# Kernel optimization log

Measured on AMD Instinct MI355X. Metric: run time of the kernel, lower is better.

Reference implementation:

```python
import jax, jax.numpy as jnp
import numpy as np

M = 100        # n_models
D = 16         # input_dim
H = 128        # hidden_dim
O = 1          # output_dim
NH = 4         # n_hidden
N = 16384      # batch of query points


def setup_inputs() -> dict:
    key = jax.random.key(0)
    ks = jax.random.split(key, 9)
    s = 0.1
    return {
        "x": jax.random.normal(ks[0], (N, D), dtype=jnp.float32),
        "W1": jax.random.normal(ks[1], (M, H, D), dtype=jnp.float32) * s,
        "b1": jax.random.normal(ks[2], (M, H), dtype=jnp.float32) * s,
        "Wh": jax.random.normal(ks[3], (M, NH, H, H), dtype=jnp.float32) * s,
        "bh": jax.random.normal(ks[4], (M, NH, H), dtype=jnp.float32) * s,
        "Wmu": jax.random.normal(ks[5], (M, O, H), dtype=jnp.float32) * s,
        "bmu": jax.random.normal(ks[6], (M, O), dtype=jnp.float32) * s,
        "Wsig": jax.random.normal(ks[7], (M, O, H), dtype=jnp.float32) * s,
        "bsig": jax.random.normal(ks[8], (M, O), dtype=jnp.float32) * s,
    }


def reference(x, W1, b1, Wh, bh, Wmu, bmu, Wsig, bsig):
    # Batched across all M models: h has shape [M, N, H]
    h = jax.nn.relu(jnp.einsum("nd,mhd->mnh", x, W1) + b1[:, None, :])
    for i in range(NH):  # fixed small structural loop over hidden layers
        h = jax.nn.relu(jnp.einsum("mnh,mkh->mnk", h, Wh[:, i]) + bh[:, i][:, None, :])
    mu = jnp.einsum("mnh,moh->mno", h, Wmu) + bmu[:, None, :]      # [M, N, O]
    sigma = jnp.exp(jnp.einsum("mnh,moh->mno", h, Wsig) + bsig[:, None, :])
    return (mu, sigma)
```

## Files before the change

### kernel.cpp

```cpp
#include <hip/hip_runtime.h>


typedef float  f32x4  __attribute__((ext_vector_type(4)));
typedef float  f32x16 __attribute__((ext_vector_type(16)));
typedef __bf16 bf16x4 __attribute__((ext_vector_type(4)));
typedef __bf16 bf16x8 __attribute__((ext_vector_type(8)));
typedef short  s16x4  __attribute__((ext_vector_type(4)));

union BF4  { bf16x4 v; uint2 u2; };
union FRAG { bf16x8 v; uint4 u4; };
union PKW  { uint2 u2; s16x4 s4; };

#define MODELS 100
#define NPT    16384
#define HDIM   128
#define SG_OFF (MODELS * NPT)

#define XB_OFF   0
#define W1B_OFF  262144
#define WHB_OFF  466944
#define WMU_OFF  7020544
#define WSG_OFF  7033344

#define GTOT 880768

__global__ __launch_bounds__(256) void cvt_weights(
    const float* __restrict__ x,   const float* __restrict__ W1,
    const float* __restrict__ Wh,  const float* __restrict__ Wmu,
    const float* __restrict__ Wsg, unsigned short* __restrict__ ws)
{
  int gid = blockIdx.x * 256 + threadIdx.x;
  if (gid >= GTOT) return;
  const float* src;
  unsigned int dst;
  if (gid < 32768) {
    src = x + gid * 8;                       dst = XB_OFF + gid * 8;
  } else if (gid < 58368) {
    int g = gid - 32768;
    src = W1 + g * 8;                        dst = W1B_OFF + g * 8;
  } else if (gid < 877568) {
    int g = gid - 58368;
    int chunk  = g >> 11;
    int within = g & 2047;
    int r   = within >> 4;
    int col = ((within & 15) * 8) ^ ((r & 15) << 3);
    src = Wh + (size_t)g * 8;
    dst = WHB_OFF + chunk * 16384 + r * HDIM + col;
  } else if (gid < 879168) {
    int g = gid - 877568;
    src = Wmu + g * 8;                       dst = WMU_OFF + g * 8;
  } else {
    int g = gid - 879168;
    src = Wsg + g * 8;                       dst = WSG_OFF + g * 8;
  }
  f32x4 a = *(const f32x4*)src;
  f32x4 b = *(const f32x4*)(src + 4);
  BF4 lo, hi;
  lo.v = __builtin_convertvector(a, bf16x4);
  hi.v = __builtin_convertvector(b, bf16x4);
  uint4 u; u.x = lo.u2.x; u.y = lo.u2.y; u.z = hi.u2.x; u.w = hi.u2.y;
  *(uint4*)&ws[dst] = u;
}

__device__ __forceinline__ void gload_lds16(const void* g, void* l) {
  __builtin_amdgcn_global_load_lds(
      (const __attribute__((address_space(1))) void*)g,
      (__attribute__((address_space(3))) void*)l, 16, 0, 0);
}

#define MFMA32(A,B,C) __builtin_amdgcn_mfma_f32_32x32x16_bf16((A),(B),(C),0,0,0)

__device__ __forceinline__ void build_hfrag(const f32x16 (&acc)[2][4],
                                            uint4 (&hf)[2][8]) {
  const s16x4 z4 = {0, 0, 0, 0};
  #pragma unroll
  for (int nt = 0; nt < 2; ++nt) {
    #pragma unroll
    for (int kt2 = 0; kt2 < 4; ++kt2) {
      uint2 P[4];
      #pragma unroll
      for (int q = 0; q < 4; ++q) {
        f32x4 v;
        v[0] = acc[nt][kt2][4*q+0]; v[1] = acc[nt][kt2][4*q+1];
        v[2] = acc[nt][kt2][4*q+2]; v[3] = acc[nt][kt2][4*q+3];
        BF4 b; b.v = __builtin_convertvector(v, bf16x4);
        PKW p; p.u2 = b.u2;
        p.s4 = __builtin_elementwise_max(p.s4, z4);
        P[q] = p.u2;
      }
      #pragma unroll
      for (int sb = 0; sb < 2; ++sb) {
        unsigned int x0 = P[2*sb].x, y0 = P[2*sb+1].x;
        unsigned int x1 = P[2*sb].y, y1 = P[2*sb+1].y;
        asm("v_permlane32_swap_b32 %0, %1" : "+v"(x0), "+v"(y0));
        asm("v_permlane32_swap_b32 %0, %1" : "+v"(x1), "+v"(y1));
        uint4 f; f.x = x0; f.y = x1; f.z = y0; f.w = y1;
        hf[nt][2*kt2+sb] = f;
      }
    }
  }
}

__global__ __launch_bounds__(256, 2) void ens_mlp(
    const unsigned short* __restrict__ ws,
    const float* __restrict__ b1,  const float* __restrict__ bh,
    const float* __restrict__ bmu, const float* __restrict__ bsg,
    float* __restrict__ out)
{
  __shared__ unsigned short wlds[2][HDIM * HDIM];

  const int bid = blockIdx.x;
  const int swz = (bid & 7) * 800 + (bid >> 3);
  const int m   = swz >> 6;
  const int nb0 = (swz & 63) << 8;

  const int t    = threadIdx.x;
  const int lane = t & 63;
  const int wv   = t >> 6;
  const int l31  = lane & 31;
  const int hi   = lane >> 5;
  const int nbw  = nb0 + wv * 64;

  const unsigned short* whm = ws + WHB_OFF + m * 65536;

  #pragma unroll
  for (int b = 0; b < 2; ++b) {
    const char* src = (const char*)(whm + b * 16384);
    char* dst = (char*)wlds[b];
    #pragma unroll
    for (int it = 0; it < 8; ++it) {
      int off = t * 16 + it * 4096;
      gload_lds16(src + off, dst + off);
    }
  }

  uint4  hfrag[2][8];
  f32x16 acc[2][4];

  {
    const unsigned short* W1m = ws + W1B_OFF + m * (HDIM * 16);
    const unsigned short* xp  = ws + XB_OFF;
    FRAG w1f[4], xf[2];
    #pragma unroll
    for (int kt2 = 0; kt2 < 4; ++kt2)
      w1f[kt2].v = *(const bf16x8*)&W1m[(kt2 * 32 + l31) * 16 + hi * 8];
    #pragma unroll
    for (int nt = 0; nt < 2; ++nt)
      xf[nt].v = *(const bf16x8*)&xp[(nbw + nt * 32 + l31) * 16 + hi * 8];
    #pragma unroll
    for (int kt2 = 0; kt2 < 4; ++kt2) {
      union { f32x16 v; f32x4 q[4]; } C;
      #pragma unroll
      for (int q = 0; q < 4; ++q)
        C.q[q] = *(const f32x4*)(b1 + m * HDIM + kt2 * 32 + q * 8 + hi * 4);
      #pragma unroll
      for (int nt = 0; nt < 2; ++nt)
        acc[nt][kt2] = MFMA32(w1f[kt2].v, xf[nt].v, C.v);
    }
  }
  build_hfrag(acc, hfrag);

  __syncthreads();

  #pragma unroll
  for (int i = 0; i < 4; ++i) {
    const char* wl = (const char*)wlds[i & 1];
    const float* bp = bh + m * 512 + i * HDIM;

    union { f32x16 v; f32x4 q[4]; } C[4];
    #pragma unroll
    for (int kt2 = 0; kt2 < 4; ++kt2)
      #pragma unroll
      for (int q = 0; q < 4; ++q)
        C[kt2].q[q] = *(const f32x4*)(bp + kt2 * 32 + q * 8 + hi * 4);

    #pragma unroll
    for (int ks = 0; ks < 8; ++ks) {
      FRAG wf[4];
      #pragma unroll
      for (int kt2 = 0; kt2 < 4; ++kt2) {
        int off = (kt2 * 32 + l31) * 256 + ((ks * 32 + hi * 16) ^ ((l31 & 15) << 4));
        wf[kt2].u4 = *(const uint4*)(wl + off);
      }
      #pragma unroll
      for (int kt2 = 0; kt2 < 4; ++kt2)
        #pragma unroll
        for (int nt = 0; nt < 2; ++nt) {
          FRAG hv; hv.u4 = hfrag[nt][ks];
          acc[nt][kt2] = MFMA32(wf[kt2].v, hv.v,
                                ks == 0 ? C[kt2].v : acc[nt][kt2]);
        }
    }
    build_hfrag(acc, hfrag);

    if (i < 3) __syncthreads();
    if (i < 2) {
      const char* src = (const char*)(whm + (i + 2) * 16384);
      char* dst = (char*)wlds[i & 1];
      #pragma unroll
      for (int it = 0; it < 8; ++it) {
        int off = t * 16 + it * 4096;
        gload_lds16(src + off, dst + off);
      }
    }
  }

  {
    FRAG hw[8];
    const unsigned short* wp = ws + (l31 == 0 ? WMU_OFF : WSG_OFF) + m * HDIM;
    #pragma unroll
    for (int ks = 0; ks < 8; ++ks) {
      if (l31 < 2) {
        hw[ks].v = *(const bf16x8*)&wp[ks * 16 + hi * 8];
      } else {
        uint4 z; z.x = 0u; z.y = 0u; z.z = 0u; z.w = 0u;
        hw[ks].u4 = z;
      }
    }
    f32x16 C;
    #pragma unroll
    for (int j = 0; j < 16; ++j) C[j] = 0.0f;
    if (hi == 0) { C[0] = bmu[m]; C[1] = bsg[m]; }

    #pragma unroll
    for (int nt = 0; nt < 2; ++nt) {
      f32x16 a2;
      #pragma unroll
      for (int ks = 0; ks < 8; ++ks) {
        FRAG hv; hv.u4 = hfrag[nt][ks];
        a2 = MFMA32(hw[ks].v, hv.v, ks == 0 ? C : a2);
      }
      if (hi == 0) {
        int n = nbw + nt * 32 + l31;
        out[m * NPT + n]          = a2[0];
        out[SG_OFF + m * NPT + n] = expf(a2[1]);
      }
    }
  }
}

extern "C" void kernel_launch(void* const* d_in, const int* in_sizes, int n_in,
                              void* d_out, int out_size, void* d_ws, size_t ws_size,
                              hipStream_t stream) {
  const float* x   = (const float*)d_in[0];
  const float* W1  = (const float*)d_in[1];
  const float* b1  = (const float*)d_in[2];
  const float* Wh  = (const float*)d_in[3];
  const float* bh  = (const float*)d_in[4];
  const float* Wmu = (const float*)d_in[5];
  const float* bmu = (const float*)d_in[6];
  const float* Wsg = (const float*)d_in[7];
  const float* bsg = (const float*)d_in[8];
  unsigned short* ws = (unsigned short*)d_ws;
  (void)in_sizes; (void)n_in; (void)out_size; (void)ws_size;

  cvt_weights<<<(GTOT + 255) / 256, 256, 0, stream>>>(x, W1, Wh, Wmu, Wsg, ws);
  ens_mlp<<<6400, 256, 0, stream>>>(ws, b1, bh, bmu, bsg, (float*)d_out);
}
```

Before: 220.6 us.

## Keep all hidden-layer weights resident: 3/4 rows in LDS, last quarter in registers

Hidden weights are repacked so that rows 0-95 of every layer go to a contiguous LDS-friendly layout and rows 96-127 to a separate region. All four layers' LDS portions are loaded once at kernel start into 96 KB of shared memory, which removes the per-layer double-buffer reloads and their __syncthreads. The remaining quarter is loaded directly into registers and double-buffered by prefetching the next layer's slice. The cost is occupancy: launch bounds drop to one block per CU because of the larger LDS footprint and higher register use, which reduces latency hiding.

```diff
diff --git a/kernel.cpp b/kernel.cpp
--- a/kernel.cpp
+++ b/kernel.cpp
@@ -18,7 +18,8 @@
 
 #define XB_OFF   0
 #define W1B_OFF  262144
-#define WHB_OFF  466944
+#define WHL_OFF  466944
+#define WHG_OFF  5382144
 #define WMU_OFF  7020544
 #define WSG_OFF  7033344
 
@@ -42,10 +43,13 @@
     int g = gid - 58368;
     int chunk  = g >> 11;
     int within = g & 2047;
-    int r   = within >> 4;
-    int col = ((within & 15) * 8) ^ ((r & 15) << 3);
+    int r = within >> 4;
+    int j = within & 15;
     src = Wh + (size_t)g * 8;
-    dst = WHB_OFF + chunk * 16384 + r * HDIM + col;
+    if (r < 96)
+      dst = WHL_OFF + chunk * 12288 + (j * 96 + r) * 8;
+    else
+      dst = WHG_OFF + chunk * 4096  + (j * 32 + (r - 96)) * 8;
   } else if (gid < 879168) {
     int g = gid - 877568;
     src = Wmu + g * 8;                       dst = WMU_OFF + g * 8;
@@ -101,13 +105,13 @@
   }
 }
 
-__global__ __launch_bounds__(256, 2) void ens_mlp(
+__global__ __launch_bounds__(256, 1) void ens_mlp(
     const unsigned short* __restrict__ ws,
     const float* __restrict__ b1,  const float* __restrict__ bh,
     const float* __restrict__ bmu, const float* __restrict__ bsg,
     float* __restrict__ out)
 {
-  __shared__ unsigned short wlds[2][HDIM * HDIM];
+  __shared__ unsigned short wlds[4 * 12288];
 
   const int bid = blockIdx.x;
   const int swz = (bid & 7) * 800 + (bid >> 3);
@@ -121,14 +125,14 @@
   const int hi   = lane >> 5;
   const int nbw  = nb0 + wv * 64;
 
-  const unsigned short* whm = ws + WHB_OFF + m * 65536;
-
-  #pragma unroll
-  for (int b = 0; b < 2; ++b) {
-    const char* src = (const char*)(whm + b * 16384);
-    char* dst = (char*)wlds[b];
-    #pragma unroll
-    for (int it = 0; it < 8; ++it) {
+  const unsigned short* whl = ws + WHL_OFF + m * 49152;
+  const unsigned short* whg = ws + WHG_OFF + m * 16384;
+
+  {
+    const char* src = (const char*)whl;
+    char* dst = (char*)wlds;
+    #pragma unroll
+    for (int it = 0; it < 24; ++it) {
       int off = t * 16 + it * 4096;
       gload_lds16(src + off, dst + off);
     }
@@ -136,6 +140,11 @@
 
   uint4  hfrag[2][8];
   f32x16 acc[2][4];
+  FRAG   gw[2][8];
+
+  #pragma unroll
+  for (int ks = 0; ks < 8; ++ks)
+    gw[0][ks].u4 = *(const uint4*)&whg[((2 * ks + hi) * 32 + l31) * 8];
 
   {
     const unsigned short* W1m = ws + W1B_OFF + m * (HDIM * 16);
@@ -164,7 +173,14 @@
 
   #pragma unroll
   for (int i = 0; i < 4; ++i) {
-    const char* wl = (const char*)wlds[i & 1];
+    if (i < 3) {
+      const unsigned short* gsrc = whg + (i + 1) * 4096;
+      #pragma unroll
+      for (int ks = 0; ks < 8; ++ks)
+        gw[(i + 1) & 1][ks].u4 = *(const uint4*)&gsrc[((2 * ks + hi) * 32 + l31) * 8];
+    }
+
+    const char* wl = (const char*)wlds + i * 24576 + (hi * 96 + l31) * 16;
     const float* bp = bh + m * 512 + i * HDIM;
 
     union { f32x16 v; f32x4 q[4]; } C[4];
@@ -176,33 +192,26 @@
 
     #pragma unroll
     for (int ks = 0; ks < 8; ++ks) {
-      FRAG wf[4];
-      #pragma unroll
-      for (int kt2 = 0; kt2 < 4; ++kt2) {
-        int off = (kt2 * 32 + l31) * 256 + ((ks * 32 + hi * 16) ^ ((l31 & 15) << 4));
-        wf[kt2].u4 = *(const uint4*)(wl + off);
-      }
-      #pragma unroll
-      for (int kt2 = 0; kt2 < 4; ++kt2)
+      FRAG wf[3];
+      #pragma unroll
+      for (int kt2 = 0; kt2 < 3; ++kt2)
+        wf[kt2].u4 = *(const uint4*)(wl + ks * 3072 + kt2 * 512);
+      #pragma unroll
+      for (int kt2 = 0; kt2 < 3; ++kt2)
         #pragma unroll
         for (int nt = 0; nt < 2; ++nt) {
           FRAG hv; hv.u4 = hfrag[nt][ks];
           acc[nt][kt2] = MFMA32(wf[kt2].v, hv.v,
                                 ks == 0 ? C[kt2].v : acc[nt][kt2]);
         }
+      #pragma unroll
+      for (int nt = 0; nt < 2; ++nt) {
+        FRAG hv; hv.u4 = hfrag[nt][ks];
+        acc[nt][3] = MFMA32(gw[i & 1][ks].v, hv.v,
+                            ks == 0 ? C[3].v : acc[nt][3]);
+      }
     }
     build_hfrag(acc, hfrag);
-
-    if (i < 3) __syncthreads();
-    if (i < 2) {
-      const char* src = (const char*)(whm + (i + 2) * 16384);
-      char* dst = (char*)wlds[i & 1];
-      #pragma unroll
-      for (int it = 0; it < 8; ++it) {
-        int off = t * 16 + it * 4096;
-        gload_lds16(src + off, dst + off);
-      }
-    }
   }
 
   {
```

New measurement: 262.6 us. 1.19x slower.
